# Optimization experiments

Hardware: AMD Instinct MI355X
Metric: run time of the kernel (lower is better)

Reference implementation:

```python
import jax, jax.numpy as jnp
import numpy as np

L, N, E, H = 1024, 8, 512, 8


def setup_inputs() -> dict:
    key = jax.random.key(0)
    k1, k2, k3, k4 = jax.random.split(key, 4)
    query = jax.random.normal(k1, (L, N, E), dtype=jnp.float32)
    time = jax.random.normal(k2, (L, N, 1), dtype=jnp.float32) * 1000.0  # timestamps
    in_proj_weight = jax.random.normal(k3, (3 * E, E), dtype=jnp.float32) * 0.02
    in_proj_bias = jnp.zeros((3 * E,), dtype=jnp.float32)
    out_proj_weight = jax.random.normal(k4, (E, E), dtype=jnp.float32) * 0.02
    out_proj_bias = jnp.zeros((E,), dtype=jnp.float32)
    return {
        "query": query,
        "time": time,
        "in_proj_weight": in_proj_weight,
        "in_proj_bias": in_proj_bias,
        "out_proj_weight": out_proj_weight,
        "out_proj_bias": out_proj_bias,
    }


def _temporal_mha(query, time, in_proj_weight, in_proj_bias, out_proj_weight, out_proj_bias):
    # Self-attention path of temporal_multi_head_attention_forward (query is key is value).
    tgt_len, bsz, embed_dim = query.shape
    num_heads = H
    head_dim = embed_dim // num_heads
    scaling = float(head_dim) ** -0.5

    # Temporal bias: tt = time.permute(1,0,2) -> (N, L, 1); alpha[b,i,j] = exp((t_bi - t_bj)/1e6)
    tt = jnp.transpose(time, (1, 0, 2))  # (N, L, 1)
    alpha_time = jnp.exp((tt - jnp.reshape(tt, (bsz, 1, tgt_len))) / 1.0e6)  # (N, L, L)

    # Fused in-projection then chunk into q, k, v.
    qkv = query @ in_proj_weight.T + in_proj_bias  # (L, N, 3E)
    q, k, v = jnp.split(qkv, 3, axis=-1)
    q = q * scaling

    def heads(x):  # (L, N, E) -> (N, H, L, hd)
        return jnp.transpose(x.reshape(tgt_len, bsz, num_heads, head_dim), (1, 2, 0, 3))

    q, k, v = heads(q), heads(k), heads(v)

    # Scores with temporal bias injected (broadcast over heads) -- this is the
    # materialized (N, H, L, L) tensor that breaks the SDPA fusion path.
    scores = jnp.einsum("bhld,bhsd->bhls", q, k) * alpha_time[:, None, :, :]
    attn = jax.nn.softmax(scores, axis=-1)  # dropout_p = 0.0 (inference/reference)

    out = jnp.einsum("bhls,bhsd->bhld", attn, v)  # (N, H, L, hd)
    out = jnp.transpose(out, (2, 0, 1, 3)).reshape(tgt_len, bsz, embed_dim)  # (L, N, E)
    return out @ out_proj_weight.T + out_proj_bias


def reference(query, time, in_proj_weight, in_proj_bias, out_proj_weight, out_proj_bias):
    return _temporal_mha(query, time, in_proj_weight, in_proj_bias, out_proj_weight, out_proj_bias)
```

## Files before the change

kernel.cpp:

```cpp
#include <hip/hip_runtime.h>
#include <cstdint>
#include <cstddef>

typedef unsigned short u16;
typedef unsigned int u32;
typedef __attribute__((ext_vector_type(8))) short short8;
typedef __attribute__((ext_vector_type(4))) float f32x4;
typedef __attribute__((ext_vector_type(16))) float f32x16;

#define L_SEQ 1024
#define N_B   8
#define E_DIM 512
#define H_H   8
#define D_H   64
#define M_ROWS 8192

#if __has_builtin(__builtin_amdgcn_exp2f)
#define EXP2(x) __builtin_amdgcn_exp2f(x)
#else
#define EXP2(x) exp2f(x)
#endif

__device__ __forceinline__ u16 f2bf(float f) {
    u32 u = __float_as_uint(f);
    u32 r = (u + 0x7fffu + ((u >> 16) & 1u)) >> 16;
    return (u16)r;
}

__device__ __forceinline__ u32 cvtpk(float lo, float hi_) {
    u32 r;
    asm("v_cvt_pk_bf16_f32 %0, %1, %2" : "=v"(r) : "v"(lo), "v"(hi_));
    return r;
}

__device__ __forceinline__ void gload16(const void* g, void* l) {
    __builtin_amdgcn_global_load_lds(
        (__attribute__((address_space(1))) void*)(g),
        (__attribute__((address_space(3))) void*)(l), 16, 0, 0);
}

__device__ __forceinline__ short8 ldsw(const u16* base, int row, int c) {
    return *reinterpret_cast<const short8*>(
        reinterpret_cast<const char*>(base) + row * 128 + ((c ^ (row & 7)) << 4));
}

__global__ __launch_bounds__(256) void convert_kernel(
    const float* __restrict__ a, const float* __restrict__ b, const float* __restrict__ c,
    u16* __restrict__ ab, u16* __restrict__ bb, u16* __restrict__ cb)
{
    const int NA = M_ROWS * E_DIM / 4;
    const int NB = 1536 * E_DIM / 4;
    const int i4 = blockIdx.x * 256 + threadIdx.x;
    const float* src; u16* dst; int j;
    if (i4 < NA)           { src = a; dst = ab; j = i4; }
    else if (i4 < NA + NB) { src = b; dst = bb; j = i4 - NA; }
    else                   { src = c; dst = cb; j = i4 - NA - NB; }
    const float4 v = reinterpret_cast<const float4*>(src)[j];
    ushort4 o;
    o.x = f2bf(v.x); o.y = f2bf(v.y); o.z = f2bf(v.z); o.w = f2bf(v.w);
    reinterpret_cast<ushort4*>(dst)[j] = o;
}

template <int MODE, int MI>
__global__ __launch_bounds__(256, 2) void gemm_kernel(
    const u16* __restrict__ A, const u16* __restrict__ B,
    const float* __restrict__ bias, const float* __restrict__ tptr,
    u16* __restrict__ qh, u16* __restrict__ kh, u16* __restrict__ vh,
    float* __restrict__ outf)
{
    constexpr int BM = MI * 32;
    __shared__ __align__(16) u16 Asm_[BM * 64];
    __shared__ __align__(16) u16 Bsm[128 * 64];
    const int tid = threadIdx.x;
    const int lane = tid & 63, w = tid >> 6;
    const int wm = w >> 1, wn = w & 1;
    const int m0 = blockIdx.x * BM, n0 = blockIdx.y * 128;

    f32x4 acc[MI][4];
    #pragma unroll
    for (int mi = 0; mi < MI; ++mi)
        #pragma unroll
        for (int ni = 0; ni < 4; ++ni)
            #pragma unroll
            for (int r = 0; r < 4; ++r) acc[mi][ni][r] = 0.f;

    const int srow = (w << 3) + (lane >> 3);
    const int csrc = ((lane & 7) ^ (lane >> 3)) << 3;

    for (int kt = 0; kt < 8; ++kt) {
        __syncthreads();
        #pragma unroll
        for (int i = 0; i < MI; ++i) {
            const int row = (i << 5) + srow;
            gload16(A + (size_t)(m0 + row) * 512 + (kt << 6) + csrc,
                    (char*)Asm_ + (i << 12) + (w << 10));
        }
        #pragma unroll
        for (int i = 0; i < 4; ++i) {
            const int row = (i << 5) + srow;
            gload16(B + (size_t)(n0 + row) * 512 + (kt << 6) + csrc,
                    (char*)Bsm + (i << 12) + (w << 10));
        }
        __syncthreads();
        #pragma unroll
        for (int k01 = 0; k01 < 2; ++k01) {
            short8 af[MI], bfr[4];
            #pragma unroll
            for (int x = 0; x < MI; ++x)
                af[x] = ldsw(Asm_, wm * (MI * 16) + (x << 4) + (lane & 15),
                             (k01 << 2) + (lane >> 4));
            #pragma unroll
            for (int x = 0; x < 4; ++x)
                bfr[x] = ldsw(Bsm, (wn << 6) + (x << 4) + (lane & 15),
                              (k01 << 2) + (lane >> 4));
            __builtin_amdgcn_s_setprio(1);
            #pragma unroll
            for (int mi = 0; mi < MI; ++mi)
                #pragma unroll
                for (int ni = 0; ni < 4; ++ni)
                    acc[mi][ni] = __builtin_amdgcn_mfma_f32_16x16x32_bf16(
                        af[mi], bfr[ni], acc[mi][ni], 0, 0, 0);
            __builtin_amdgcn_s_setprio(0);
        }
    }

    const int nb = n0 + (wn << 6) + (lane & 15);
    const int mb = m0 + wm * (MI * 16) + ((lane >> 4) << 2);
    float bsv[4];
    #pragma unroll
    for (int ni = 0; ni < 4; ++ni) bsv[ni] = bias[nb + (ni << 4)];
    const int sec = n0 >> 9;

    #pragma unroll
    for (int mi = 0; mi < MI; ++mi) {
        #pragma unroll
        for (int r = 0; r < 4; ++r) {
            const int m = mb + (mi << 4) + r;
            float scale = 1.f;
            if (MODE == 0) {
                if (sec == 0)      scale = 0.18033688f * __expf(tptr[m] * 1e-6f);
                else if (sec == 1) scale = __expf(tptr[m] * -1e-6f);
            }
            #pragma unroll
            for (int ni = 0; ni < 4; ++ni) {
                const int n = nb + (ni << 4);
                const float v = acc[mi][ni][r] + bsv[ni];
                if (MODE == 0) {
                    const int l_seq = m >> 3, bb2 = m & 7;
                    const int hh = (n & 511) >> 6, dd = n & 63;
                    u16* dst = (sec == 0) ? qh : (sec == 1) ? kh : vh;
                    dst[(((size_t)(bb2 << 3) + hh) * L_SEQ + l_seq) * D_H + dd] = f2bf(v * scale);
                } else {
                    outf[(size_t)m * 512 + n] = v;
                }
            }
        }
    }
}

__global__ __launch_bounds__(256) void transpose_v(
    const u16* __restrict__ vh, u16* __restrict__ vt)
{
    __shared__ __align__(16) u16 T[64 * 64];
    const int bh = blockIdx.x, kt = blockIdx.y;
    const u16* src = vh + ((size_t)bh * L_SEQ + kt * 64) * D_H;

    #pragma unroll
    for (int rnd = 0; rnd < 2; ++rnd) {
        const int slot = rnd * 256 + threadIdx.x;
        const int row = slot >> 3, c = slot & 7;
        const uint4 v = *reinterpret_cast<const uint4*>(src + row * 64 + c * 8);
        const int cs = c ^ (row & 7) ^ ((row >> 3) & 7);
        *reinterpret_cast<uint4*>(&T[row * 64 + cs * 8]) = v;
    }
    __syncthreads();
    #pragma unroll
    for (int rnd = 0; rnd < 2; ++rnd) {
        const int slot = rnd * 256 + threadIdx.x;
        const int d = slot >> 3, kc = slot & 7;
        u16 tmp[8];
        #pragma unroll
        for (int j = 0; j < 8; ++j) {
            const int row = kc * 8 + j;
            const int col = (((d >> 3) ^ (row & 7) ^ ((row >> 3) & 7)) << 3) + (d & 7);
            tmp[j] = T[row * 64 + col];
        }
        *reinterpret_cast<uint4*>(vt + ((size_t)bh * D_H + d) * L_SEQ + kt * 64 + kc * 8) =
            *reinterpret_cast<uint4*>(tmp);
    }
}

__global__ __launch_bounds__(128) void attn_kernel(
    const u16* __restrict__ qh, const u16* __restrict__ kh,
    const u16* __restrict__ vt, u16* __restrict__ ao)
{
    __shared__ __align__(16) u16 SM[16384];

    const int tid = threadIdx.x;
    const int lane = tid & 63, w = tid >> 6;
    const int hi = lane >> 5, q31 = lane & 31;
    const int bh = blockIdx.x, qt = blockIdx.y;
    const int b = bh >> 3, h = bh & 7;

    const u16* qrow = qh + ((size_t)bh * L_SEQ + qt * 64 + w * 32 + q31) * D_H;
    short8 qf[4];
    #pragma unroll
    for (int ks = 0; ks < 4; ++ks)
        qf[ks] = *reinterpret_cast<const short8*>(qrow + ks * 16 + hi * 8);

    f32x16 oacc[2];
    #pragma unroll
    for (int d = 0; d < 2; ++d)
        #pragma unroll
        for (int r = 0; r < 16; ++r) oacc[d][r] = 0.f;
    float l_run = 0.f;

    const u16* kbase = kh + (size_t)bh * L_SEQ * D_H;
    const u16* vbase = vt + (size_t)bh * D_H * L_SEQ;
    const int r8 = lane >> 3;
    const int csrc = ((lane & 7) ^ r8) << 3;

    auto stage = [&](int buf, int kt) {
        #pragma unroll
        for (int i = 0; i < 4; ++i) {
            const int row = (w << 5) + (i << 3) + r8;
            gload16(kbase + (size_t)(kt * 64 + row) * 64 + csrc,
                    (char*)SM + buf * 8192 + (w << 12) + (i << 10));
            gload16(vbase + (size_t)row * 1024 + kt * 64 + csrc,
                    (char*)SM + 16384 + buf * 8192 + (w << 12) + (i << 10));
        }
    };

    int cur = 0;
    stage(0, 0);
    __syncthreads();

    for (int kt = 0; kt < 16; ++kt) {
        if (kt < 15) stage(cur ^ 1, kt + 1);
        const u16* Kc = SM + cur * 4096;
        const u16* Vc = SM + 8192 + cur * 4096;

        f32x16 s[2];
        #pragma unroll
        for (int d = 0; d < 2; ++d)
            #pragma unroll
            for (int r = 0; r < 16; ++r) s[d][r] = 0.f;
        __builtin_amdgcn_s_setprio(1);
        #pragma unroll
        for (int ks = 0; ks < 4; ++ks) {
            const int c = 2 * ks + hi;
            const short8 ka0 = ldsw(Kc, q31, c);
            const short8 ka1 = ldsw(Kc, 32 + q31, c);
            s[0] = __builtin_amdgcn_mfma_f32_32x32x16_bf16(ka0, qf[ks], s[0], 0, 0, 0);
            s[1] = __builtin_amdgcn_mfma_f32_32x32x16_bf16(ka1, qf[ks], s[1], 0, 0, 0);
        }
        __builtin_amdgcn_s_setprio(0);

        float a0 = 0.f, a1 = 0.f, a2 = 0.f, a3 = 0.f;
        #pragma unroll
        for (int hh = 0; hh < 2; ++hh)
            #pragma unroll
            for (int r = 0; r < 16; r += 4) {
                s[hh][r + 0] = EXP2(s[hh][r + 0]); a0 += s[hh][r + 0];
                s[hh][r + 1] = EXP2(s[hh][r + 1]); a1 += s[hh][r + 1];
                s[hh][r + 2] = EXP2(s[hh][r + 2]); a2 += s[hh][r + 2];
                s[hh][r + 3] = EXP2(s[hh][r + 3]); a3 += s[hh][r + 3];
            }
        l_run += (a0 + a1) + (a2 + a3);

        __builtin_amdgcn_s_setprio(1);
        #pragma unroll
        for (int ks = 0; ks < 4; ++ks) {
            const int e = ks & 1, hh = ks >> 1;
            const u32 pkA = cvtpk(s[hh][8 * e + 0], s[hh][8 * e + 1]);
            const u32 pkB = cvtpk(s[hh][8 * e + 2], s[hh][8 * e + 3]);
            const u32 pkC = cvtpk(s[hh][8 * e + 4], s[hh][8 * e + 5]);
            const u32 pkD = cvtpk(s[hh][8 * e + 6], s[hh][8 * e + 7]);
            const u32 keep0 = hi ? pkC : pkA, keep1 = hi ? pkD : pkB;
            const u32 send0 = hi ? pkA : pkC, send1 = hi ? pkB : pkD;
            const u32 r0 = (u32)__shfl_xor((int)send0, 32);
            const u32 r1 = (u32)__shfl_xor((int)send1, 32);
            union { u32 u[4]; short8 v; } pf;
            pf.u[0] = hi ? r0 : keep0;  pf.u[1] = hi ? r1 : keep1;
            pf.u[2] = hi ? keep0 : r0;  pf.u[3] = hi ? keep1 : r1;
            const int c = 2 * ks + hi;
            const short8 va0 = ldsw(Vc, q31, c);
            const short8 va1 = ldsw(Vc, 32 + q31, c);
            oacc[0] = __builtin_amdgcn_mfma_f32_32x32x16_bf16(va0, pf.v, oacc[0], 0, 0, 0);
            oacc[1] = __builtin_amdgcn_mfma_f32_32x32x16_bf16(va1, pf.v, oacc[1], 0, 0, 0);
        }
        __builtin_amdgcn_s_setprio(0);
        __syncthreads();
        cur ^= 1;
    }

    const float l_tot = l_run + __shfl_xor(l_run, 32);
    const float inv = 1.f / l_tot;
    float* myO = (float*)SM + w * 2080;
    #pragma unroll
    for (int dh = 0; dh < 2; ++dh)
        #pragma unroll
        for (int r = 0; r < 16; ++r) {
            const int d = dh * 32 + (r & 3) + 8 * (r >> 2) + 4 * hi;
            myO[q31 * 65 + d] = oacc[dh][r] * inv;
        }
    __syncthreads();
    #pragma unroll
    for (int i = 0; i < 4; ++i) {
        const int slot = i * 64 + lane;
        const int qq = slot >> 3, dc = slot & 7;
        u16 outv[8];
        #pragma unroll
        for (int j = 0; j < 8; ++j) outv[j] = f2bf(myO[qq * 65 + dc * 8 + j]);
        const int lrow = qt * 64 + w * 32 + qq;
        *reinterpret_cast<uint4*>(ao + ((size_t)lrow * N_B + b) * E_DIM + h * 64 + dc * 8) =
            *reinterpret_cast<uint4*>(outv);
    }
}

extern "C" void kernel_launch(void* const* d_in, const int* in_sizes, int n_in,
                              void* d_out, int out_size, void* d_ws, size_t ws_size,
                              hipStream_t stream) {
    const float* query = (const float*)d_in[0];
    const float* timep = (const float*)d_in[1];
    const float* w_in  = (const float*)d_in[2];
    const float* b_in  = (const float*)d_in[3];
    const float* w_out = (const float*)d_in[4];
    const float* b_out = (const float*)d_in[5];
    float* out = (float*)d_out;

    u16* ws = (u16*)d_ws;
    const size_t SZ = (size_t)M_ROWS * E_DIM;
    u16* Abf  = ws;
    u16* Wibf = Abf + SZ;
    u16* Wobf = Wibf + 1536 * 512;
    u16* qhb  = Wobf + 512 * 512;
    u16* khb  = qhb + SZ;
    u16* vhb  = khb + SZ;
    u16* vtb  = vhb + SZ;
    u16* aob  = vtb + SZ;

    convert_kernel<<<5120, 256, 0, stream>>>(query, w_in, w_out, Abf, Wibf, Wobf);
    gemm_kernel<0, 4><<<dim3(64, 12), 256, 0, stream>>>(
        Abf, Wibf, b_in, timep, qhb, khb, vhb, nullptr);
    transpose_v<<<dim3(64, 16), 256, 0, stream>>>(vhb, vtb);
    attn_kernel<<<dim3(64, 16), 128, 0, stream>>>(qhb, khb, vtb, aob);
    gemm_kernel<1, 2><<<dim3(128, 4), 256, 0, stream>>>(
        aob, Wobf, b_out, nullptr, nullptr, nullptr, nullptr, out);
}
```

Baseline: 138.5 us.

## Software-pipeline PV matmul one tile behind QK with triple-buffered V

Defers the P·V MFMA for each key tile to the next iteration, issuing it right after the next tile's QK MFMAs so the exp/softmax and pack work can overlap with matrix-core work. V staging moves to a three-slot ring in LDS (larger shared allocation) so the previous tile's V stays resident while the next is loaded, and a tail block finishes the last tile. The cost is extra registers holding the packed probabilities and more LDS, which may reduce occupancy.

New measurement: 142.2 us. +2.6%, slower.

```diff
diff --git a/kernel.cpp b/kernel.cpp
--- a/kernel.cpp
+++ b/kernel.cpp
@@ -194,7 +194,7 @@
     const u16* __restrict__ qh, const u16* __restrict__ kh,
     const u16* __restrict__ vt, u16* __restrict__ ao)
 {
-    __shared__ __align__(16) u16 SM[16384];
+    __shared__ __align__(16) u16 SM[20480];
 
     const int tid = threadIdx.x;
     const int lane = tid & 63, w = tid >> 6;
@@ -220,14 +220,15 @@
     const int r8 = lane >> 3;
     const int csrc = ((lane & 7) ^ r8) << 3;
 
-    auto stage = [&](int buf, int kt) {
+    auto stage = [&](int kbuf, int kt) {
+        const int vslot = (kt + 2) % 3;
         #pragma unroll
         for (int i = 0; i < 4; ++i) {
             const int row = (w << 5) + (i << 3) + r8;
             gload16(kbase + (size_t)(kt * 64 + row) * 64 + csrc,
-                    (char*)SM + buf * 8192 + (w << 12) + (i << 10));
+                    (char*)SM + kbuf * 8192 + (w << 12) + (i << 10));
             gload16(vbase + (size_t)row * 1024 + kt * 64 + csrc,
-                    (char*)SM + 16384 + buf * 8192 + (w << 12) + (i << 10));
+                    (char*)SM + 16384 + vslot * 8192 + (w << 12) + (i << 10));
         }
     };
 
@@ -235,10 +236,11 @@
     stage(0, 0);
     __syncthreads();
 
+    u32 pfp[4][4];
+
     for (int kt = 0; kt < 16; ++kt) {
         if (kt < 15) stage(cur ^ 1, kt + 1);
         const u16* Kc = SM + cur * 4096;
-        const u16* Vc = SM + 8192 + cur * 4096;
 
         f32x16 s[2];
         #pragma unroll
@@ -253,6 +255,20 @@
             const short8 ka1 = ldsw(Kc, 32 + q31, c);
             s[0] = __builtin_amdgcn_mfma_f32_32x32x16_bf16(ka0, qf[ks], s[0], 0, 0, 0);
             s[1] = __builtin_amdgcn_mfma_f32_32x32x16_bf16(ka1, qf[ks], s[1], 0, 0, 0);
+        }
+        if (kt > 0) {
+            const u16* Vp = SM + 8192 + ((kt + 1) % 3) * 4096;
+            #pragma unroll
+            for (int ks = 0; ks < 4; ++ks) {
+                const int c = 2 * ks + hi;
+                const short8 va0 = ldsw(Vp, q31, c);
+                const short8 va1 = ldsw(Vp, 32 + q31, c);
+                union { u32 u[4]; short8 v; } pv_;
+                pv_.u[0] = pfp[ks][0]; pv_.u[1] = pfp[ks][1];
+                pv_.u[2] = pfp[ks][2]; pv_.u[3] = pfp[ks][3];
+                oacc[0] = __builtin_amdgcn_mfma_f32_32x32x16_bf16(va0, pv_.v, oacc[0], 0, 0, 0);
+                oacc[1] = __builtin_amdgcn_mfma_f32_32x32x16_bf16(va1, pv_.v, oacc[1], 0, 0, 0);
+            }
         }
         __builtin_amdgcn_s_setprio(0);
 
@@ -268,7 +284,6 @@
             }
         l_run += (a0 + a1) + (a2 + a3);
 
-        __builtin_amdgcn_s_setprio(1);
         #pragma unroll
         for (int ks = 0; ks < 4; ++ks) {
             const int e = ks & 1, hh = ks >> 1;
@@ -280,18 +295,28 @@
             const u32 send0 = hi ? pkA : pkC, send1 = hi ? pkB : pkD;
             const u32 r0 = (u32)__shfl_xor((int)send0, 32);
             const u32 r1 = (u32)__shfl_xor((int)send1, 32);
-            union { u32 u[4]; short8 v; } pf;
-            pf.u[0] = hi ? r0 : keep0;  pf.u[1] = hi ? r1 : keep1;
-            pf.u[2] = hi ? keep0 : r0;  pf.u[3] = hi ? keep1 : r1;
-            const int c = 2 * ks + hi;
-            const short8 va0 = ldsw(Vc, q31, c);
-            const short8 va1 = ldsw(Vc, 32 + q31, c);
-            oacc[0] = __builtin_amdgcn_mfma_f32_32x32x16_bf16(va0, pf.v, oacc[0], 0, 0, 0);
-            oacc[1] = __builtin_amdgcn_mfma_f32_32x32x16_bf16(va1, pf.v, oacc[1], 0, 0, 0);
-        }
-        __builtin_amdgcn_s_setprio(0);
+            pfp[ks][0] = hi ? r0 : keep0;  pfp[ks][1] = hi ? r1 : keep1;
+            pfp[ks][2] = hi ? keep0 : r0;  pfp[ks][3] = hi ? keep1 : r1;
+        }
         __syncthreads();
         cur ^= 1;
+    }
+
+    {
+        const u16* Vp = SM + 8192 + 2 * 4096;
+        __builtin_amdgcn_s_setprio(1);
+        #pragma unroll
+        for (int ks = 0; ks < 4; ++ks) {
+            const int c = 2 * ks + hi;
+            const short8 va0 = ldsw(Vp, q31, c);
+            const short8 va1 = ldsw(Vp, 32 + q31, c);
+            union { u32 u[4]; short8 v; } pv_;
+            pv_.u[0] = pfp[ks][0]; pv_.u[1] = pfp[ks][1];
+            pv_.u[2] = pfp[ks][2]; pv_.u[3] = pfp[ks][3];
+            oacc[0] = __builtin_amdgcn_mfma_f32_32x32x16_bf16(va0, pv_.v, oacc[0], 0, 0, 0);
+            oacc[1] = __builtin_amdgcn_mfma_f32_32x32x16_bf16(va1, pv_.v, oacc[1], 0, 0, 0);
+        }
+        __builtin_amdgcn_s_setprio(0);
     }
 
     const float l_tot = l_run + __shfl_xor(l_run, 32);
```
